# Performance work log

Measured on AMD Instinct MI355X. Metric: run time of the kernel, lower is better.

Reference implementation:

```python
import jax, jax.numpy as jnp
import numpy as np


def setup_inputs() -> dict:
    key = jax.random.key(0)
    k1, k2 = jax.random.split(key)
    data = jax.random.normal(k1, (1000000, 64), dtype=jnp.float32)
    # unique, in-range indices (ONNX ScatterND is undefined for duplicates)
    indices = jnp.arange(100000, dtype=jnp.int64 if jax.config.jax_enable_x64 else jnp.int32).reshape(100000, 1)
    updates = jax.random.normal(k2, (100000, 64), dtype=jnp.float32)
    return {"data": data, "indices": indices, "updates": updates}


def reference(data, indices, updates):
    # ONNX ScatterND with k = indices.shape[-1] = 1: scatter rows of `updates`
    # into a copy of `data` at row positions indices[..., 0].
    rows = indices[..., 0]  # [num_updates]
    return data.at[rows].set(updates)
```

## Files before the change

kernel.cpp:

```cpp
#include <hip/hip_runtime.h>
#include <stdint.h>


typedef float f32x4 __attribute__((ext_vector_type(4)));
typedef uint32_t u32x4 __attribute__((ext_vector_type(4)));

__global__ __launch_bounds__(256) void zero_flags_kernel(
    u32x4* __restrict__ p, size_t n16) {
    const size_t i = (size_t)blockIdx.x * blockDim.x + threadIdx.x;
    if (i < n16) p[i] = (u32x4){0u, 0u, 0u, 0u};
}

__global__ __launch_bounds__(256) void scatter_flag_kernel(
    const int* __restrict__ idx,
    const f32x4* __restrict__ upd,
    f32x4* __restrict__ out,
    uint8_t* __restrict__ flags,
    size_t total4) {
    const size_t i = (size_t)blockIdx.x * blockDim.x + threadIdx.x;
    if (i < total4) {
        const size_t row = i >> 4;
        const size_t col = i & 15;
        const int r = idx[row];
        out[(size_t)r * 16 + col] = upd[i];
        if (col == 0) flags[r] = 1;
    }
}

__global__ __launch_bounds__(256) void copy_skip_kernel(
    const f32x4* __restrict__ src,
    f32x4* __restrict__ dst,
    const uint8_t* __restrict__ flags,
    size_t n4) {
    const size_t i = (size_t)blockIdx.x * blockDim.x + threadIdx.x;
    if (i < n4 && !flags[i >> 4]) dst[i] = src[i];
}

__global__ __launch_bounds__(256) void copy_flat_kernel(
    const f32x4* __restrict__ src, f32x4* __restrict__ dst, size_t n4) {
    const size_t i = (size_t)blockIdx.x * blockDim.x + threadIdx.x;
    if (i < n4) dst[i] = src[i];
}

__global__ __launch_bounds__(256) void scatter_flat_kernel(
    const int* __restrict__ idx,
    const f32x4* __restrict__ upd,
    f32x4* __restrict__ out,
    size_t total4) {
    const size_t i = (size_t)blockIdx.x * blockDim.x + threadIdx.x;
    if (i < total4) {
        const size_t row = i >> 4;
        const size_t col = i & 15;
        const int r = idx[row];
        out[(size_t)r * 16 + col] = upd[i];
    }
}

extern "C" void kernel_launch(void* const* d_in, const int* in_sizes, int n_in,
                              void* d_out, int out_size, void* d_ws, size_t ws_size,
                              hipStream_t stream) {
    const float* data    = (const float*)d_in[0];
    const int*   indices = (const int*)d_in[1];
    const float* updates = (const float*)d_in[2];
    float* out = (float*)d_out;

    const size_t n4          = (size_t)out_size / 4;
    const size_t num_rows    = (size_t)out_size / 64;
    const size_t num_updates = (size_t)in_sizes[2] / 64;
    const size_t total4      = num_updates * 16;

    const int block = 256;
    auto blocks_for = [&](size_t work) {
        return (int)((work + block - 1) / block);
    };

    if (ws_size >= num_rows && (num_rows % 16) == 0) {
        uint8_t* flags = (uint8_t*)d_ws;
        const size_t n16 = num_rows / 16;
        zero_flags_kernel<<<blocks_for(n16), block, 0, stream>>>(
            (u32x4*)flags, n16);
        scatter_flag_kernel<<<blocks_for(total4), block, 0, stream>>>(
            indices, (const f32x4*)updates, (f32x4*)out, flags, total4);
        copy_skip_kernel<<<blocks_for(n4), block, 0, stream>>>(
            (const f32x4*)data, (f32x4*)out, flags, n4);
    } else {
        copy_flat_kernel<<<blocks_for(n4), block, 0, stream>>>(
            (const f32x4*)data, (f32x4*)out, n4);
        scatter_flat_kernel<<<blocks_for(total4), block, 0, stream>>>(
            indices, (const f32x4*)updates, (f32x4*)out, total4);
    }
}
```

Measured before the change: 99.20 us.

## Split flag setting into small kernel and fuse scatter with skip-copy

Flag marking moves into its own small kernel with one thread per update row. The row scatter and the flag-guarded copy of untouched rows are then merged into one grid, where the leading threads scatter updates and the remaining threads copy data. This cuts the tail and launch gap between the large scatter and copy passes, at the cost of an extra tiny launch. The fused path is used only when the scatter work is a multiple of the block size, so each block does one kind of work.

```diff
diff --git a/kernel.cpp b/kernel.cpp
--- a/kernel.cpp
+++ b/kernel.cpp
@@ -11,29 +11,30 @@
     if (i < n16) p[i] = (u32x4){0u, 0u, 0u, 0u};
 }
 
-__global__ __launch_bounds__(256) void scatter_flag_kernel(
+__global__ __launch_bounds__(256) void flag_scatter_kernel(
+    const int* __restrict__ idx, uint8_t* __restrict__ flags, int n) {
+    const int t = blockIdx.x * blockDim.x + threadIdx.x;
+    if (t < n) flags[idx[t]] = 1;
+}
+
+__global__ __launch_bounds__(256) void mega_kernel(
+    const f32x4* __restrict__ data,
+    const f32x4* __restrict__ upd,
     const int* __restrict__ idx,
-    const f32x4* __restrict__ upd,
+    const uint8_t* __restrict__ flags,
     f32x4* __restrict__ out,
-    uint8_t* __restrict__ flags,
-    size_t total4) {
+    size_t total4,
+    size_t n4) {
     const size_t i = (size_t)blockIdx.x * blockDim.x + threadIdx.x;
     if (i < total4) {
         const size_t row = i >> 4;
         const size_t col = i & 15;
         const int r = idx[row];
         out[(size_t)r * 16 + col] = upd[i];
-        if (col == 0) flags[r] = 1;
+    } else {
+        const size_t j = i - total4;
+        if (j < n4 && !flags[j >> 4]) out[j] = data[j];
     }
-}
-
-__global__ __launch_bounds__(256) void copy_skip_kernel(
-    const f32x4* __restrict__ src,
-    f32x4* __restrict__ dst,
-    const uint8_t* __restrict__ flags,
-    size_t n4) {
-    const size_t i = (size_t)blockIdx.x * blockDim.x + threadIdx.x;
-    if (i < n4 && !flags[i >> 4]) dst[i] = src[i];
 }
 
 __global__ __launch_bounds__(256) void copy_flat_kernel(
@@ -43,10 +44,8 @@
 }
 
 __global__ __launch_bounds__(256) void scatter_flat_kernel(
-    const int* __restrict__ idx,
-    const f32x4* __restrict__ upd,
-    f32x4* __restrict__ out,
-    size_t total4) {
+    const int* __restrict__ idx, const f32x4* __restrict__ upd,
+    f32x4* __restrict__ out, size_t total4) {
     const size_t i = (size_t)blockIdx.x * blockDim.x + threadIdx.x;
     if (i < total4) {
         const size_t row = i >> 4;
@@ -74,15 +73,16 @@
         return (int)((work + block - 1) / block);
     };
 
-    if (ws_size >= num_rows && (num_rows % 16) == 0) {
+    if (ws_size >= num_rows && (num_rows % 16) == 0 && (total4 % block) == 0) {
         uint8_t* flags = (uint8_t*)d_ws;
         const size_t n16 = num_rows / 16;
         zero_flags_kernel<<<blocks_for(n16), block, 0, stream>>>(
             (u32x4*)flags, n16);
-        scatter_flag_kernel<<<blocks_for(total4), block, 0, stream>>>(
-            indices, (const f32x4*)updates, (f32x4*)out, flags, total4);
-        copy_skip_kernel<<<blocks_for(n4), block, 0, stream>>>(
-            (const f32x4*)data, (f32x4*)out, flags, n4);
+        flag_scatter_kernel<<<blocks_for(num_updates), block, 0, stream>>>(
+            indices, flags, (int)num_updates);
+        mega_kernel<<<blocks_for(total4 + n4), block, 0, stream>>>(
+            (const f32x4*)data, (const f32x4*)updates, indices, flags,
+            (f32x4*)out, total4, n4);
     } else {
         copy_flat_kernel<<<blocks_for(n4), block, 0, stream>>>(
             (const f32x4*)data, (f32x4*)out, n4);
```

Result: no change. 98.74 us (-0.5%).
